# Performance work log

Hardware: AMD Instinct MI355X
Metric: run time of the kernel (lower is better)

## Reference

```python
import jax, jax.numpy as jnp
import numpy as np
import math

B, S, D, H = 8, 1024, 1024, 16
HD = D // H  # head_features = 64
SCALE = math.sqrt(HD)


def setup_inputs() -> dict:
    key = jax.random.key(0)
    k0, k1, k2, k3, k4 = jax.random.split(key, 5)
    x = jax.random.normal(k0, (B, S, D), dtype=jnp.float32)
    attn_mask = (jax.random.uniform(k1, (B, S, S)) < 0.9).astype(jnp.float32)
    w_scale = 1.0 / math.sqrt(D)  # keep unsafe exp in finite range
    Wq = jax.random.normal(k2, (D, D), dtype=jnp.float32) * w_scale
    Wk = jax.random.normal(k3, (D, D), dtype=jnp.float32) * w_scale
    Wv = jax.random.normal(k4, (D, D), dtype=jnp.float32) * w_scale
    return {"x": x, "attn_mask": attn_mask, "Wq": Wq, "Wk": Wk, "Wv": Wv}


def reference(x, attn_mask, Wq, Wk, Wv):
    b, s, _ = x.shape

    def split_heads(t):  # [b,s,D] -> [b,H,s,HD]
        return t.reshape(b, s, H, HD).transpose(0, 2, 1, 3)

    q = split_heads(x @ Wq)
    k = split_heads(x @ Wk)
    v = split_heads(x @ Wv)

    # unsafe softmax: exp without max subtraction, multiplicative mask, +1e-8 denom
    scores = jnp.einsum('bhsd,bhtd->bhst', q, k) / SCALE
    e = jnp.exp(scores) * attn_mask[:, None, :, :]
    w = e / (e.sum(axis=3, keepdims=True) + 1e-8)

    ctx = jnp.einsum('bhst,bhtd->bhsd', w, v)  # [b,H,s,HD]
    return ctx.transpose(0, 2, 1, 3).reshape(b, s, D)
```

## Files before the change

kernel.cpp:

```cpp
#include <hip/hip_runtime.h>

#define KDIM 1024

typedef _Float16 half8 __attribute__((ext_vector_type(8)));
typedef _Float16 half4 __attribute__((ext_vector_type(4)));
typedef __fp16 fp16x2 __attribute__((ext_vector_type(2)));
typedef __fp16 fp16x4 __attribute__((ext_vector_type(4)));
typedef float f32x4 __attribute__((ext_vector_type(4)));

#if defined(__has_builtin)
#if __has_builtin(__builtin_amdgcn_global_load_lds)
#define HAVE_GLDS 1
#endif
#if __has_builtin(__builtin_amdgcn_exp2f)
#define EXP2(x) __builtin_amdgcn_exp2f(x)
#endif
#if __has_builtin(__builtin_amdgcn_cvt_pkrtz)
#define HAVE_PKRTZ 1
#endif
#if __has_builtin(__builtin_amdgcn_fdot2)
#define HAVE_FDOT2 1
#endif
#endif
#ifndef EXP2
#define EXP2(x) exp2f(x)
#endif

__device__ __forceinline__ void stage16(const _Float16* g, _Float16* wave_base, int lane) {
#ifdef HAVE_GLDS
  __builtin_amdgcn_global_load_lds(
      (const __attribute__((address_space(1))) void*)g,
      (__attribute__((address_space(3))) void*)wave_base, 16, 0, 0);
#else
  *(half8*)(wave_base + lane * 8) = *(const half8*)g;
#endif
}

#define BARRIER() __builtin_amdgcn_s_barrier()
#define LGKM0()                                         \
  do {                                                  \
    asm volatile("s_waitcnt lgkmcnt(0)" ::: "memory");  \
    __builtin_amdgcn_sched_barrier(0);                  \
  } while (0)
#define VMCNT(n)                                               \
  do {                                                         \
    asm volatile("s_waitcnt vmcnt(" #n ")" ::: "memory");      \
  } while (0)

__global__ void prep_kernel(const float* __restrict__ x, const float* __restrict__ am,
                            const float* __restrict__ Wq, const float* __restrict__ Wk,
                            const float* __restrict__ Wv, _Float16* __restrict__ xb,
                            _Float16* __restrict__ Wqkvt, unsigned long long* __restrict__ bits) {
  __shared__ _Float16 tile[32][33];
  int bid = blockIdx.x;
  if (bid < 8192) {
    size_t i = ((size_t)bid * 256 + threadIdx.x) * 4;
    float4 v = *(const float4*)(x + i);
    half4 h = { (_Float16)v.x, (_Float16)v.y, (_Float16)v.z, (_Float16)v.w };
    *(half4*)(xb + i) = h;
  } else if (bid < 11264) {
    int zz = bid - 8192;
    int z = zz >> 10;
    int rem = zz & 1023;
    int bx = rem & 31, by = rem >> 5;
    const float* src = z == 0 ? Wq : (z == 1 ? Wk : Wv);
    _Float16* dst = Wqkvt + (size_t)z * KDIM * KDIM;
    float sc = (z == 0) ? 0.18033688011112042f : 1.0f;
    int tx = threadIdx.x & 31, ty = threadIdx.x >> 5;
    int c0 = bx * 32, r0 = by * 32;
#pragma unroll
    for (int i = 0; i < 4; i++) {
      int r = r0 + ty + i * 8;
      tile[tx][ty + i * 8] = (_Float16)(src[(size_t)r * KDIM + c0 + tx] * sc);
    }
    __syncthreads();
#pragma unroll
    for (int i = 0; i < 4; i++) {
      int n = c0 + ty + i * 8;
      dst[(size_t)n * KDIM + r0 + tx] = tile[ty + i * 8][tx];
    }
  } else {
    size_t i = (size_t)(bid - 11264) * 256 + threadIdx.x;
    unsigned long long b = __ballot(am[i] != 0.0f);
    if ((threadIdx.x & 63) == 0) bits[i >> 6] = b;
  }
}

__global__ __launch_bounds__(512, 2)
void gemm_kernel(const _Float16* __restrict__ A, const _Float16* __restrict__ Bt,
                 _Float16* __restrict__ Qt, _Float16* __restrict__ Kh,
                 _Float16* __restrict__ Vth) {
  __shared__ _Float16 As[2 * 16384];
  __shared__ _Float16 Bs[2 * 12288];
  int tid = threadIdx.x;
  int lane = tid & 63, w = tid >> 6;
  int la = lane & 15, qd = lane >> 4;
  int wm = w & 1, wn = w >> 1;
  int bid = blockIdx.x;
  int wg = (bid & 7) * 64 + (bid >> 3);
  int by = wg >> 4, bx = wg & 15;
  int m0 = by * 256, n0 = bx * 192;
  int srow = tid >> 3;
  int scc = ((srow & 7) ^ (tid & 7)) << 3;
  const int rc0 = ((qd ^ (la & 7)) << 3);
  const int rc1 = (((4 | qd) ^ (la & 7)) << 3);

  const _Float16* Ab = A + (size_t)m0 * KDIM;
  const _Float16* Bb = Bt + (size_t)n0 * KDIM;

  const _Float16* pA0a = Ab + (size_t)(srow) * KDIM + scc;
  const _Float16* pA0b = Ab + (size_t)(srow + 64) * KDIM + scc;
  const _Float16* pA1a = Ab + (size_t)(srow + 128) * KDIM + scc;
  const _Float16* pA1b = Ab + (size_t)(srow + 192) * KDIM + scc;
  const _Float16* pB0 = Bb + (size_t)(srow) * KDIM + scc;
  const _Float16* pB1 = Bb + (size_t)(srow + 64) * KDIM + scc;
  const _Float16* pB2 = Bb + (size_t)(srow + 128) * KDIM + scc;

  _Float16* ldsAw = As + w * 512;
  _Float16* ldsBw = Bs + w * 512;

  const _Float16* baseA0 = As + wm * 4096 + la * 64 + rc0;
  const _Float16* baseA1 = As + wm * 4096 + la * 64 + rc1;
  const _Float16* baseB0 = Bs + (wn * 16 + la) * 64 + rc0;
  const _Float16* baseB1 = Bs + (wn * 16 + la) * 64 + rc1;

  f32x4 acc[8][3] = {};
  half8 af[4][2], bf0[2], bf1[2], bf2[2];

#define STAGE_A0(B)                                       \
  do {                                                    \
    stage16(pA0a, ldsAw + (B) * 16384, lane);             \
    stage16(pA0b, ldsAw + (B) * 16384 + 4096, lane);      \
    pA0a += 64; pA0b += 64;                               \
  } while (0)
#define STAGE_A1(B)                                       \
  do {                                                    \
    stage16(pA1a, ldsAw + (B) * 16384 + 8192, lane);      \
    stage16(pA1b, ldsAw + (B) * 16384 + 12288, lane);     \
    pA1a += 64; pA1b += 64;                               \
  } while (0)
#define STAGE_B0(B)                                       \
  do { stage16(pB0, ldsBw + (B) * 12288, lane); pB0 += 64; } while (0)
#define STAGE_B1(B)                                       \
  do { stage16(pB1, ldsBw + (B) * 12288 + 4096, lane); pB1 += 64; } while (0)
#define STAGE_B2(B)                                       \
  do { stage16(pB2, ldsBw + (B) * 12288 + 8192, lane); pB2 += 64; } while (0)
#define LD_AF(CUR, MH)                                                               \
  do {                                                                               \
    _Pragma("unroll") for (int mi = 0; mi < 4; ++mi) {                               \
      af[mi][0] = *(const half8*)(baseA0 + (CUR) * 16384 + (MH) * 8192 + mi * 1024); \
      af[mi][1] = *(const half8*)(baseA1 + (CUR) * 16384 + (MH) * 8192 + mi * 1024); \
    }                                                                                \
  } while (0)
#define LD_B(BF, CUR, NJ)                                                  \
  do {                                                                     \
    BF[0] = *(const half8*)(baseB0 + (CUR) * 12288 + (NJ) * 4096);         \
    BF[1] = *(const half8*)(baseB1 + (CUR) * 12288 + (NJ) * 4096);         \
  } while (0)
#define MFMA_N(MH, NJ, BF)                                                          \
  do {                                                                              \
    _Pragma("unroll") for (int mi = 0; mi < 4; ++mi) {                              \
      acc[(MH) * 4 + mi][NJ] = __builtin_amdgcn_mfma_f32_16x16x32_f16(              \
          af[mi][0], BF[0], acc[(MH) * 4 + mi][NJ], 0, 0, 0);                       \
      acc[(MH) * 4 + mi][NJ] = __builtin_amdgcn_mfma_f32_16x16x32_f16(              \
          af[mi][1], BF[1], acc[(MH) * 4 + mi][NJ], 0, 0, 0);                       \
    }                                                                               \
  } while (0)

  STAGE_A0(0); STAGE_B0(0); STAGE_A1(0); STAGE_B1(0); STAGE_B2(0);
  VMCNT(0);
  BARRIER();

#define KTILE(T, CUR, NXT)                                     \
  do {                                                         \
    int t = (T);                                               \
                                                  \
    LD_AF(CUR, 0);                                             \
    LD_B(bf0, CUR, 0);                                         \
    if (t < 15) { STAGE_A0(NXT); STAGE_B0(NXT); }              \
    BARRIER();                                                 \
    LGKM0();                                                   \
    __builtin_amdgcn_s_setprio(1);                             \
    MFMA_N(0, 0, bf0);                                         \
    __builtin_amdgcn_s_setprio(0);                             \
    if (t < 15) { VMCNT(3); } else { VMCNT(0); }               \
    BARRIER();                                                 \
                                                  \
    LD_B(bf1, CUR, 1);                                         \
    LD_B(bf2, CUR, 2);                                         \
    if (t < 15) STAGE_A1(NXT);                                 \
    BARRIER();                                                 \
    LGKM0();                                                   \
    __builtin_amdgcn_s_setprio(1);                             \
    MFMA_N(0, 1, bf1);                                         \
    MFMA_N(0, 2, bf2);                                         \
    __builtin_amdgcn_s_setprio(0);                             \
    BARRIER();                                                 \
                                                  \
    LD_AF(CUR, 1);                                             \
    if (t < 15) { STAGE_B1(NXT); STAGE_B2(NXT); }              \
    BARRIER();                                                 \
    LGKM0();                                                   \
    __builtin_amdgcn_s_setprio(1);                             \
    MFMA_N(1, 0, bf0);                                         \
    MFMA_N(1, 1, bf1);                                         \
    MFMA_N(1, 2, bf2);                                         \
    __builtin_amdgcn_s_setprio(0);                             \
    if (t < 15) { VMCNT(4); }                                  \
    BARRIER();                                                 \
  } while (0)

#pragma unroll 1
  for (int tp = 0; tp < 8; ++tp) {
    KTILE(2 * tp, 0, 1);
    KTILE(2 * tp + 1, 1, 0);
  }

#undef KTILE
#undef MFMA_N
#undef LD_B
#undef LD_AF
#undef STAGE_B2
#undef STAGE_B1
#undef STAGE_B0
#undef STAGE_A1
#undef STAGE_A0

  int rr = lane >> 2, c4 = lane & 3;
  _Float16* ep = As + w * 1280;
#pragma unroll
  for (int mh = 0; mh < 2; ++mh) {
    int srow0 = m0 + mh * 128 + wm * 64;
    int b = srow0 >> 10, s0 = srow0 & 1023;
#pragma unroll
    for (int nj = 0; nj < 3; ++nj) {
      int colh = n0 + wn * 16 + nj * 64;
      int whichf = colh >> 10;
      int cm = colh & 1023;
      int hh = cm >> 6, d0 = cm & 63;
      if (whichf == 1) {
        _Float16* kb = Kh + (size_t)(b * 16 + hh) * 1024 * 64;
#pragma unroll
        for (int mi = 0; mi < 4; ++mi) {
          f32x4 v = acc[mh * 4 + mi][nj];
          int s = s0 + mi * 16 + qd * 4;
#pragma unroll
          for (int rg = 0; rg < 4; ++rg)
            kb[(size_t)(s + rg) * 64 + d0 + la] = (_Float16)v[rg];
        }
      } else {
        _Float16* dst = (whichf == 0) ? Qt : Vth;
#pragma unroll
        for (int mi = 0; mi < 4; ++mi) {
          f32x4 v = acc[mh * 4 + mi][nj];
          half4 hv = { (_Float16)v[0], (_Float16)v[1], (_Float16)v[2], (_Float16)v[3] };
          *(half4*)(ep + la * 72 + mi * 16 + qd * 4) = hv;
        }
        half8 o0 = *(const half8*)(ep + rr * 72 + c4 * 16);
        half8 o1 = *(const half8*)(ep + rr * 72 + c4 * 16 + 8);
        _Float16* gp = dst + ((size_t)(b * 16 + hh) * 64 + d0 + rr) * 1024 + s0 + c4 * 16;
        *(half8*)gp = o0;
        *(half8*)(gp + 8) = o1;
      }
    }
  }
}

__global__ __launch_bounds__(512, 2)
void attn_kernel(const _Float16* __restrict__ Qt, const _Float16* __restrict__ K,
                 const _Float16* __restrict__ Vt, const unsigned long long* __restrict__ mbits,
                 float* __restrict__ out) {
  __shared__ _Float16 Ks[2][2 * 64 * 32];
  __shared__ _Float16 Vs[2][2 * 64 * 40];
  int tid = threadIdx.x;
  int lane = tid & 63, w4 = tid >> 6;
  int la = lane & 15, qd = lane >> 4;
  int linear = blockIdx.x;
  int xlo = linear & 7;
  int tmp = linear >> 3;
  int qt = tmp & 3;
  int hb = (tmp >> 2) * 8 + xlo;
  int h = hb & 15, b = hb >> 4;
  const _Float16* Qp = Qt + (size_t)hb * 64 * 1024;
  const _Float16* Kp = K + (size_t)hb * 1024 * 64;
  const _Float16* Vp = Vt + (size_t)hb * 64 * 1024;
  int q0w = qt * 256 + w4 * 16;
  half8 qf[2][2];
#pragma unroll
  for (int qi = 0; qi < 2; qi++)
#pragma unroll
    for (int ks = 0; ks < 2; ks++)
#pragma unroll
      for (int j = 0; j < 8; j++)
        qf[qi][ks][j] = Qp[(size_t)(ks * 32 + qd * 8 + j) * 1024 + q0w + qi * 128 + la];
  unsigned long long mq[2][4];
#pragma unroll
  for (int qi = 0; qi < 2; qi++) {
    const ulonglong2* mp =
        (const ulonglong2*)(mbits + ((size_t)b * 1024 + q0w + qi * 128 + la) * 16 + qd * 4);
    ulonglong2 m01 = mp[0];
    ulonglong2 m23 = mp[1];
    mq[qi][0] = m01.x; mq[qi][1] = m01.y; mq[qi][2] = m23.x; mq[qi][3] = m23.y;
  }
  f32x4 acco[2][4] = {};
  float rs[2] = {0.f, 0.f};
  int kt_t = (tid & 255) >> 2;
  int kt_d = (tid >> 8) * 32 + (((tid & 3) ^ ((tid >> 2) & 3) ^ ((tid >> 4) & 3)) << 3);
  int kc8 = ((qd ^ (la & 3) ^ (la >> 2)) << 3);
  int vd = tid >> 3;
  int vt = (tid & 7) * 8;
  int vs_off = (vt >= 32 ? 2560 : 0) + vd * 40 + (vt & 31);
#if defined(HAVE_FDOT2) && defined(HAVE_PKRTZ)
  fp16x2 one2 = { (__fp16)1.0f, (__fp16)1.0f };
#endif
  {
    stage16(Kp + (size_t)kt_t * 64 + kt_d, Ks[0] + w4 * 512, lane);
    half8 vv = *(const half8*)(Vp + (size_t)vd * 1024 + vt);
    *(half8*)(Vs[0] + vs_off) = vv;
  }
  __syncthreads();
  for (int tt = 0; tt < 16; tt++) {
    int cur = tt & 1, nxt = cur ^ 1;
    half8 vvn;
    if (tt < 15) {
      vvn = *(const half8*)(Vp + (size_t)vd * 1024 + (tt + 1) * 64 + vt);
      stage16(Kp + (size_t)((tt + 1) * 64 + kt_t) * 64 + kt_d, Ks[nxt] + w4 * 512, lane);
    }
    const _Float16* ks_ = Ks[cur];
    const _Float16* vs_ = Vs[cur];
    unsigned long long mw0 = __shfl(mq[0][tt & 3], ((tt >> 2) << 4) + la);
    unsigned long long mw1 = __shfl(mq[1][tt & 3], ((tt >> 2) << 4) + la);
#pragma unroll
    for (int tsub = 0; tsub < 4; tsub++) {
      half8 kf0 = *(const half8*)(ks_ + (tsub * 16 + la) * 32 + kc8);
      half8 kf1 = *(const half8*)(ks_ + 2048 + (tsub * 16 + la) * 32 + kc8);
      f32x4 a0 = {}, a1 = {};
      a0 = __builtin_amdgcn_mfma_f32_16x16x32_f16(kf0, qf[0][0], a0, 0, 0, 0);
      a1 = __builtin_amdgcn_mfma_f32_16x16x32_f16(kf0, qf[1][0], a1, 0, 0, 0);
      a0 = __builtin_amdgcn_mfma_f32_16x16x32_f16(kf1, qf[0][1], a0, 0, 0, 0);
      a1 = __builtin_amdgcn_mfma_f32_16x16x32_f16(kf1, qf[1][1], a1, 0, 0, 0);
      half4 pf[2];
#pragma unroll
      for (int qi = 0; qi < 2; qi++) {
        const f32x4& aa = qi ? a1 : a0;
        unsigned long long mw = qi ? mw1 : mw0;
        float e0 = ((mw >> (tsub * 16 + qd * 4 + 0)) & 1ull) ? EXP2(aa[0]) : 0.0f;
        float e1 = ((mw >> (tsub * 16 + qd * 4 + 1)) & 1ull) ? EXP2(aa[1]) : 0.0f;
        float e2 = ((mw >> (tsub * 16 + qd * 4 + 2)) & 1ull) ? EXP2(aa[2]) : 0.0f;
        float e3 = ((mw >> (tsub * 16 + qd * 4 + 3)) & 1ull) ? EXP2(aa[3]) : 0.0f;
#ifdef HAVE_PKRTZ
        fp16x2 p01 = __builtin_amdgcn_cvt_pkrtz(e0, e1);
        fp16x2 p23 = __builtin_amdgcn_cvt_pkrtz(e2, e3);
        fp16x4 pfv = __builtin_shufflevector(p01, p23, 0, 1, 2, 3);
        pf[qi] = __builtin_bit_cast(half4, pfv);
#else
        pf[qi][0] = (_Float16)e0; pf[qi][1] = (_Float16)e1;
        pf[qi][2] = (_Float16)e2; pf[qi][3] = (_Float16)e3;
#endif
#if defined(HAVE_FDOT2) && defined(HAVE_PKRTZ)
        rs[qi] = __builtin_amdgcn_fdot2(p01, one2, rs[qi], false);
        rs[qi] = __builtin_amdgcn_fdot2(p23, one2, rs[qi], false);
#else
        rs[qi] += e0 + e1 + e2 + e3;
#endif
      }
#pragma unroll
      for (int nsub = 0; nsub < 4; nsub++) {
        half4 vf = *(const half4*)(vs_ + (tsub >> 1) * 2560 + (nsub * 16 + la) * 40 +
                                   (tsub & 1) * 16 + qd * 4);
        acco[0][nsub] = __builtin_amdgcn_mfma_f32_16x16x16f16(pf[0], vf, acco[0][nsub], 0, 0, 0);
        acco[1][nsub] = __builtin_amdgcn_mfma_f32_16x16x16f16(pf[1], vf, acco[1][nsub], 0, 0, 0);
      }
    }
    if (tt < 15) *(half8*)(Vs[nxt] + vs_off) = vvn;
    __syncthreads();
  }
  float* op = out + (size_t)b * 1024 * 1024 + (size_t)h * 64;
#pragma unroll
  for (int qi = 0; qi < 2; qi++) {
    float r0 = rs[qi];
    r0 += __shfl_xor(r0, 16);
    r0 += __shfl_xor(r0, 32);
    float inv_q = 1.0f / (r0 + 1e-8f);
#pragma unroll
    for (int rg = 0; rg < 4; rg++) {
      float inv = __shfl(inv_q, qd * 4 + rg);
      int s = q0w + qi * 128 + qd * 4 + rg;
#pragma unroll
      for (int nsub = 0; nsub < 4; nsub++)
        op[(size_t)s * 1024 + nsub * 16 + la] = acco[qi][nsub][rg] * inv;
    }
  }
}

extern "C" void kernel_launch(void* const* d_in, const int* in_sizes, int n_in,
                              void* d_out, int out_size, void* d_ws, size_t ws_size,
                              hipStream_t stream) {
  (void)in_sizes; (void)n_in; (void)out_size; (void)ws_size;
  const float* x = (const float*)d_in[0];
  const float* am = (const float*)d_in[1];
  const float* Wq = (const float*)d_in[2];
  const float* Wk = (const float*)d_in[3];
  const float* Wv = (const float*)d_in[4];
  float* out = (float*)d_out;

  char* p = (char*)d_ws;
  _Float16* xb = (_Float16*)p;    p += (size_t)8192 * 1024 * 2;
  _Float16* Wqkvt = (_Float16*)p; p += (size_t)3 * 1024 * 1024 * 2;
  _Float16* Qt = (_Float16*)p;    p += (size_t)8192 * 1024 * 2;
  _Float16* Kh = (_Float16*)p;    p += (size_t)8192 * 1024 * 2;
  _Float16* Vth = (_Float16*)p;   p += (size_t)8192 * 1024 * 2;
  unsigned long long* mb = (unsigned long long*)p;

  prep_kernel<<<44032, 256, 0, stream>>>(x, am, Wq, Wk, Wv, xb, Wqkvt, mb);
  gemm_kernel<<<dim3(512), 512, 0, stream>>>(xb, Wqkvt, Qt, Kh, Vth);
  attn_kernel<<<512, 512, 0, stream>>>(Qt, Kh, Vth, mb, out);
}
```

Baseline: 249.8 us.

## Deepen K prefetch to two tiles ahead with fine-grained waitcnt barriers

Grows the K shared-memory ring from 2 to 4 buffers and issues the K tile two iterations ahead. The full __syncthreads is replaced by explicit s_waitcnt vmcnt(1) plus a barrier, so the newest K load can stay in flight across iterations. It also raises wave priority around the MFMA groups and pre-shifts the mask words so each tile extracts a single nibble. The cost is more LDS per block, which could hurt occupancy at two blocks per CU, and the hand-counted vmcnt values depend on the compiler's load order.

```diff
diff --git a/kernel.cpp b/kernel.cpp
--- a/kernel.cpp
+++ b/kernel.cpp
@@ -270,7 +270,7 @@
 void attn_kernel(const _Float16* __restrict__ Qt, const _Float16* __restrict__ K,
                  const _Float16* __restrict__ Vt, const unsigned long long* __restrict__ mbits,
                  float* __restrict__ out) {
-  __shared__ _Float16 Ks[2][2 * 64 * 32];
+  __shared__ _Float16 Ks[4][2 * 64 * 32];
   __shared__ _Float16 Vs[2][2 * 64 * 40];
   int tid = threadIdx.x;
   int lane = tid & 63, w4 = tid >> 6;
@@ -314,40 +314,48 @@
   fp16x2 one2 = { (__fp16)1.0f, (__fp16)1.0f };
 #endif
   {
+    half8 vv0 = *(const half8*)(Vp + (size_t)vd * 1024 + vt);
+    __builtin_amdgcn_sched_barrier(0);
     stage16(Kp + (size_t)kt_t * 64 + kt_d, Ks[0] + w4 * 512, lane);
-    half8 vv = *(const half8*)(Vp + (size_t)vd * 1024 + vt);
-    *(half8*)(Vs[0] + vs_off) = vv;
-  }
-  __syncthreads();
+    stage16(Kp + (size_t)(64 + kt_t) * 64 + kt_d, Ks[1] + w4 * 512, lane);
+    *(half8*)(Vs[0] + vs_off) = vv0;
+  }
+  asm volatile("s_waitcnt vmcnt(1) lgkmcnt(0)" ::: "memory");
+  BARRIER();
   for (int tt = 0; tt < 16; tt++) {
-    int cur = tt & 1, nxt = cur ^ 1;
+    const _Float16* ks_ = Ks[tt & 3];
+    const _Float16* vs_ = Vs[tt & 1];
     half8 vvn;
     if (tt < 15) {
       vvn = *(const half8*)(Vp + (size_t)vd * 1024 + (tt + 1) * 64 + vt);
-      stage16(Kp + (size_t)((tt + 1) * 64 + kt_t) * 64 + kt_d, Ks[nxt] + w4 * 512, lane);
-    }
-    const _Float16* ks_ = Ks[cur];
-    const _Float16* vs_ = Vs[cur];
+      __builtin_amdgcn_sched_barrier(0);
+    }
+    if (tt < 14)
+      stage16(Kp + (size_t)((tt + 2) * 64 + kt_t) * 64 + kt_d, Ks[(tt + 2) & 3] + w4 * 512, lane);
     unsigned long long mw0 = __shfl(mq[0][tt & 3], ((tt >> 2) << 4) + la);
     unsigned long long mw1 = __shfl(mq[1][tt & 3], ((tt >> 2) << 4) + la);
+    unsigned long long mq0s = mw0 >> (qd * 4);
+    unsigned long long mq1s = mw1 >> (qd * 4);
 #pragma unroll
     for (int tsub = 0; tsub < 4; tsub++) {
       half8 kf0 = *(const half8*)(ks_ + (tsub * 16 + la) * 32 + kc8);
       half8 kf1 = *(const half8*)(ks_ + 2048 + (tsub * 16 + la) * 32 + kc8);
       f32x4 a0 = {}, a1 = {};
+      __builtin_amdgcn_s_setprio(1);
       a0 = __builtin_amdgcn_mfma_f32_16x16x32_f16(kf0, qf[0][0], a0, 0, 0, 0);
       a1 = __builtin_amdgcn_mfma_f32_16x16x32_f16(kf0, qf[1][0], a1, 0, 0, 0);
       a0 = __builtin_amdgcn_mfma_f32_16x16x32_f16(kf1, qf[0][1], a0, 0, 0, 0);
       a1 = __builtin_amdgcn_mfma_f32_16x16x32_f16(kf1, qf[1][1], a1, 0, 0, 0);
+      __builtin_amdgcn_s_setprio(0);
       half4 pf[2];
 #pragma unroll
       for (int qi = 0; qi < 2; qi++) {
         const f32x4& aa = qi ? a1 : a0;
-        unsigned long long mw = qi ? mw1 : mw0;
-        float e0 = ((mw >> (tsub * 16 + qd * 4 + 0)) & 1ull) ? EXP2(aa[0]) : 0.0f;
-        float e1 = ((mw >> (tsub * 16 + qd * 4 + 1)) & 1ull) ? EXP2(aa[1]) : 0.0f;
-        float e2 = ((mw >> (tsub * 16 + qd * 4 + 2)) & 1ull) ? EXP2(aa[2]) : 0.0f;
-        float e3 = ((mw >> (tsub * 16 + qd * 4 + 3)) & 1ull) ? EXP2(aa[3]) : 0.0f;
+        unsigned nib = (unsigned)((qi ? mq1s : mq0s) >> (tsub * 16)) & 15u;
+        float e0 = (nib & 1u) ? EXP2(aa[0]) : 0.0f;
+        float e1 = (nib & 2u) ? EXP2(aa[1]) : 0.0f;
+        float e2 = (nib & 4u) ? EXP2(aa[2]) : 0.0f;
+        float e3 = (nib & 8u) ? EXP2(aa[3]) : 0.0f;
 #ifdef HAVE_PKRTZ
         fp16x2 p01 = __builtin_amdgcn_cvt_pkrtz(e0, e1);
         fp16x2 p23 = __builtin_amdgcn_cvt_pkrtz(e2, e3);
@@ -368,12 +376,20 @@
       for (int nsub = 0; nsub < 4; nsub++) {
         half4 vf = *(const half4*)(vs_ + (tsub >> 1) * 2560 + (nsub * 16 + la) * 40 +
                                    (tsub & 1) * 16 + qd * 4);
+        __builtin_amdgcn_s_setprio(1);
         acco[0][nsub] = __builtin_amdgcn_mfma_f32_16x16x16f16(pf[0], vf, acco[0][nsub], 0, 0, 0);
         acco[1][nsub] = __builtin_amdgcn_mfma_f32_16x16x16f16(pf[1], vf, acco[1][nsub], 0, 0, 0);
+        __builtin_amdgcn_s_setprio(0);
       }
     }
-    if (tt < 15) *(half8*)(Vs[nxt] + vs_off) = vvn;
-    __syncthreads();
+    if (tt < 15) *(half8*)(Vs[(tt + 1) & 1] + vs_off) = vvn;
+    if (tt < 14) {
+      asm volatile("s_waitcnt vmcnt(1) lgkmcnt(0)" ::: "memory");
+      BARRIER();
+    } else if (tt == 14) {
+      asm volatile("s_waitcnt vmcnt(0) lgkmcnt(0)" ::: "memory");
+      BARRIER();
+    }
   }
   float* op = out + (size_t)b * 1024 * 1024 + (size_t)h * 64;
 #pragma unroll
```

New measurement: 247.6 us. No clear change (-0.9%).
